# Kernel optimization log

Measured on AMD Instinct MI355X. Metric: run time of the kernel, lower is better.

## Reference

```python
import jax, jax.numpy as jnp
import numpy as np

V, C, H, L, E, D, B, T = 32000, 1024, 16, 3, 8, 1024, 8, 512
FF = 4 * C
EPS = 1e-5


def setup_inputs() -> dict:
    key = jax.random.key(0)
    ks = iter(jax.random.split(key, 32))
    def w(shape, s=0.02):
        return jax.random.normal(next(ks), shape, jnp.float32) * s
    return {
        "idx": jax.random.randint(next(ks), (B, T), 0, V),
        "tok_emb": w((V, C)),
        "ln1_g": jnp.ones((L, C)), "ln1_b": jnp.zeros((L, C)),
        "ln2_g": jnp.ones((L, C)), "ln2_b": jnp.zeros((L, C)),
        "qkv_w": w((L, C, 3 * C)), "proj_w": w((L, C, C)),
        "ff_w1": w((L, C, FF)), "ff_b1": jnp.zeros((L, FF)),
        "ff_w2": w((L, FF, C)), "ff_b2": jnp.zeros((L, C)),
        "router_w": w((C, E)),
        "exp_w1": w((E, C, D)), "exp_b1": jnp.zeros((E, D)),
        "exp_w2": w((E, D, C)), "exp_b2": jnp.zeros((E, C)),
        "lnf_g": jnp.ones((C,)), "lnf_b": jnp.zeros((C,)),
        "head_w": w((C, V)),
    }


def layernorm(x, g, b):
    m = x.mean(-1, keepdims=True)
    v = x.var(-1, keepdims=True)
    return (x - m) * jax.lax.rsqrt(v + EPS) * g + b


def rope_cos_sin(t, d):
    inv = 1.0 / (10000.0 ** (jnp.arange(0, d, 2, dtype=jnp.float32) / d))
    fr = jnp.arange(t, dtype=jnp.float32)[:, None] * inv[None, :]  # [T, d/2]
    emb = jnp.concatenate([fr, fr], -1)  # [T, d]
    return jnp.cos(emb), jnp.sin(emb)


def rot_half(x):
    x1, x2 = jnp.split(x, 2, axis=-1)
    return jnp.concatenate([-x2, x1], -1)


def attn(x, qkv_w, proj_w):
    b, t, c = x.shape
    d = c // H
    qkv = (x @ qkv_w).reshape(b, t, 3, H, d).transpose(2, 0, 3, 1, 4)  # [3,B,H,T,d]
    q, k, v = qkv[0], qkv[1], qkv[2]
    cos, sin = rope_cos_sin(t, d)
    q = q * cos + rot_half(q) * sin
    k = k * cos + rot_half(k) * sin
    s = jnp.einsum('bhqd,bhkd->bhqk', q, k) / np.float32(np.sqrt(d))
    causal = jnp.tril(jnp.ones((t, t), bool))
    s = jnp.where(causal, s, jnp.float32(-1e30))
    a = jax.nn.softmax(s, -1)
    y = jnp.einsum('bhqk,bhkd->bhqd', a, v)
    y = y.transpose(0, 2, 1, 3).reshape(b, t, c)
    return y @ proj_w


def moe(xf, router_w, exp_w1, exp_b1, exp_w2, exp_b2):
    # router softmax -> top-2 -> renormalize -> scatter into dense [N,E] mask
    probs = jax.nn.softmax(xf @ router_w, -1)
    tw, ti = jax.lax.top_k(probs, 2)
    tw = tw / tw.sum(-1, keepdims=True)
    n = xf.shape[0]
    mask = jnp.zeros((n, E), xf.dtype).at[jnp.arange(n)[:, None], ti].set(tw)
    # per-expert dense FFN over all tokens, combined with sparse weights
    h = jax.nn.gelu(jnp.einsum('nc,ecd->end', xf, exp_w1) + exp_b1[:, None, :], approximate=False)
    y = jnp.einsum('end,edc->enc', h, exp_w2) + exp_b2[:, None, :]
    return jnp.einsum('ne,enc->nc', mask, y)


def reference(idx, tok_emb, ln1_g, ln1_b, ln2_g, ln2_b, qkv_w, proj_w,
              ff_w1, ff_b1, ff_w2, ff_b2, router_w, exp_w1, exp_b1,
              exp_w2, exp_b2, lnf_g, lnf_b, head_w):
    x = tok_emb[idx]  # [B,T,C]
    for l in range(L):
        x = x + attn(layernorm(x, ln1_g[l], ln1_b[l]), qkv_w[l], proj_w[l])
        h = layernorm(x, ln2_g[l], ln2_b[l])
        x = x + (jax.nn.gelu(h @ ff_w1[l] + ff_b1[l], approximate=False) @ ff_w2[l] + ff_b2[l])
    b, t, c = x.shape
    x = moe(x.reshape(b * t, c), router_w, exp_w1, exp_b1, exp_w2, exp_b2).reshape(b, t, c)
    x = layernorm(x, lnf_g, lnf_b)
    return x @ head_w  # logits [B,T,V]
```

## Files before the change

kernel.cpp:

```cpp
#include <hip/hip_runtime.h>
#include <math.h>


#define NTOK  4096
#define CDIM  1024
#define HEADS 16
#define DHEAD 64
#define LAYERS 3
#define NEXP  8
#define DEXP  1024
#define TSEQ  512
#define FFDIM 4096
#define VOCAB 32000
#define C3    3072

typedef __attribute__((ext_vector_type(8))) short short8;
typedef __attribute__((ext_vector_type(4))) float f32x4;

__device__ __forceinline__ unsigned short f2bf(float f) {
  unsigned int u = __builtin_bit_cast(unsigned int, f);
  return (unsigned short)((u + 0x7fffu + ((u >> 16) & 1u)) >> 16);
}
__device__ __forceinline__ float bf2f(unsigned short h) {
  return __builtin_bit_cast(float, ((unsigned int)h) << 16);
}

__global__ __launch_bounds__(256) void embed_kernel(const int* __restrict__ idx,
                                                    const float* __restrict__ emb,
                                                    float* __restrict__ x) {
  int i = blockIdx.x * 256 + threadIdx.x;
  int n = i >> 8, c4 = i & 255;
  const float4* src = (const float4*)(emb + (size_t)idx[n] * CDIM);
  ((float4*)(x + (size_t)n * CDIM))[c4] = src[c4];
}

__global__ void rope_table_kernel(float* __restrict__ ct, float* __restrict__ st) {
  int t = blockIdx.x, p = threadIdx.x;
  float inv = powf(10000.0f, -(float)p / 32.0f);
  float ang = (float)t * inv;
  ct[t * 32 + p] = cosf(ang);
  st[t * 32 + p] = sinf(ang);
}

__global__ __launch_bounds__(256) void qkv_prep_kernel(
    const float* __restrict__ qkv, const float* __restrict__ ct,
    const float* __restrict__ st,
    unsigned short* __restrict__ Qh, unsigned short* __restrict__ Qm,
    unsigned short* __restrict__ Ql,
    unsigned short* __restrict__ Kh, unsigned short* __restrict__ Km,
    unsigned short* __restrict__ Kl,
    unsigned short* __restrict__ Vth, unsigned short* __restrict__ Vtm,
    unsigned short* __restrict__ Vtl) {
  __shared__ unsigned short sVh[64 * 64], sVm[64 * 64], sVl[64 * 64];
  const int tid = threadIdx.x;
  const int tt0 = blockIdx.x * 64, h = blockIdx.y, b = blockIdx.z;
  const int bh = b * HEADS + h;
#pragma unroll
  for (int u = 0; u < 8; u++) {
    int pidx = tid + u * 256;
    int tl = pidx >> 5, p = pidx & 31;
    int t = tt0 + tl;
    size_t nb = ((size_t)(b * TSEQ + t)) * C3 + h * DHEAD;
    float c0 = ct[t * 32 + p], s0 = st[t * 32 + p];
    size_t ob = ((size_t)bh * TSEQ + t) * 64;
    float a = qkv[nb + p], bb = qkv[nb + p + 32];
    float lo = a * c0 - bb * s0, hi = bb * c0 + a * s0;
    unsigned short w0, w1;
    float r;
    w0 = f2bf(lo); r = lo - bf2f(w0); w1 = f2bf(r); r -= bf2f(w1);
    Qh[ob + p] = w0; Qm[ob + p] = w1; Ql[ob + p] = f2bf(r);
    w0 = f2bf(hi); r = hi - bf2f(w0); w1 = f2bf(r); r -= bf2f(w1);
    Qh[ob + p + 32] = w0; Qm[ob + p + 32] = w1; Ql[ob + p + 32] = f2bf(r);
    a = qkv[nb + CDIM + p]; bb = qkv[nb + CDIM + p + 32];
    lo = a * c0 - bb * s0; hi = bb * c0 + a * s0;
    w0 = f2bf(lo); r = lo - bf2f(w0); w1 = f2bf(r); r -= bf2f(w1);
    Kh[ob + p] = w0; Km[ob + p] = w1; Kl[ob + p] = f2bf(r);
    w0 = f2bf(hi); r = hi - bf2f(w0); w1 = f2bf(r); r -= bf2f(w1);
    Kh[ob + p + 32] = w0; Km[ob + p + 32] = w1; Kl[ob + p + 32] = f2bf(r);
  }
#pragma unroll
  for (int u = 0; u < 4; u++) {
    int vidx = tid + u * 256;
    int tl = vidx >> 4, d4 = (vidx & 15) * 4;
    int t = tt0 + tl;
    float4 v = *(const float4*)(qkv + ((size_t)(b * TSEQ + t)) * C3 + 2 * CDIM + h * DHEAD + d4);
    float vv[4] = {v.x, v.y, v.z, v.w};
#pragma unroll
    for (int j = 0; j < 4; j++) {
      unsigned short w0 = f2bf(vv[j]);
      float r = vv[j] - bf2f(w0);
      unsigned short w1 = f2bf(r);
      r -= bf2f(w1);
      sVh[(d4 + j) * 64 + tl] = w0;
      sVm[(d4 + j) * 64 + tl] = w1;
      sVl[(d4 + j) * 64 + tl] = f2bf(r);
    }
  }
  __syncthreads();
#pragma unroll
  for (int u = 0; u < 2; u++) {
    int idx = tid + u * 256;
    int d = idx >> 3, seg = (idx & 7) * 8;
    size_t go = ((size_t)bh * 64 + d) * TSEQ + tt0 + seg;
    *(short8*)(Vth + go) = *(const short8*)(sVh + d * 64 + seg);
    *(short8*)(Vtm + go) = *(const short8*)(sVm + d * 64 + seg);
    *(short8*)(Vtl + go) = *(const short8*)(sVl + d * 64 + seg);
  }
}

__global__ __launch_bounds__(256) void flash_attn_kernel(
    const unsigned short* __restrict__ Qh, const unsigned short* __restrict__ Qm,
    const unsigned short* __restrict__ Ql,
    const unsigned short* __restrict__ Kh, const unsigned short* __restrict__ Km,
    const unsigned short* __restrict__ Kl,
    const unsigned short* __restrict__ Vth, const unsigned short* __restrict__ Vtm,
    const unsigned short* __restrict__ Vtl,
    unsigned short* __restrict__ ath, unsigned short* __restrict__ atl) {
  __shared__ __align__(16) unsigned short sK[3][2][64 * 32];
  __shared__ __align__(16) unsigned short sV[3][2][64 * 32];
  __shared__ __align__(16) unsigned short sP[3][2][4][16 * 32];
  const int tid = threadIdx.x;
  const int wv = tid >> 6, ln = tid & 63;
  const int qt = blockIdx.x, h = blockIdx.y, b = blockIdx.z;
  const int bh = b * HEADS + h;
  const int lr = ln & 15, lg = ln >> 4;
  const int q0 = qt * 64 + wv * 16;

  const size_t qoff = ((size_t)bh * TSEQ + q0 + lr) * 64 + 8 * lg;
  short8 qf[3][2];
  qf[0][0] = *(const short8*)(Qh + qoff); qf[0][1] = *(const short8*)(Qh + qoff + 32);
  qf[1][0] = *(const short8*)(Qm + qoff); qf[1][1] = *(const short8*)(Qm + qoff + 32);
  qf[2][0] = *(const short8*)(Ql + qoff); qf[2][1] = *(const short8*)(Ql + qoff + 32);

  f32x4 Y[4];
#pragma unroll
  for (int j = 0; j < 4; j++) Y[j] = (f32x4){0.f, 0.f, 0.f, 0.f};
  float m[4] = {-1e30f, -1e30f, -1e30f, -1e30f};
  float l[4] = {0.f, 0.f, 0.f, 0.f};

  const int r0 = tid >> 3, sg = (tid & 7) * 8;
  const int half = sg >> 5, soff = (sg & 31);

  for (int kt = 0; kt <= qt; kt++) {
    const int kb = kt * 64;
    short8 stg[12];
#pragma unroll
    for (int u = 0; u < 2; u++) {
      int row = r0 + 32 * u;
      size_t gk = ((size_t)bh * TSEQ + kb + row) * 64 + sg;
      size_t gv = ((size_t)bh * 64 + row) * TSEQ + kb + sg;
      stg[u * 6 + 0] = *(const short8*)(Kh + gk);
      stg[u * 6 + 1] = *(const short8*)(Km + gk);
      stg[u * 6 + 2] = *(const short8*)(Kl + gk);
      stg[u * 6 + 3] = *(const short8*)(Vth + gv);
      stg[u * 6 + 4] = *(const short8*)(Vtm + gv);
      stg[u * 6 + 5] = *(const short8*)(Vtl + gv);
    }
    __syncthreads();
#pragma unroll
    for (int u = 0; u < 2; u++) {
      int off = (r0 + 32 * u) * 32 + soff;
      *(short8*)(&sK[0][half][off]) = stg[u * 6 + 0];
      *(short8*)(&sK[1][half][off]) = stg[u * 6 + 1];
      *(short8*)(&sK[2][half][off]) = stg[u * 6 + 2];
      *(short8*)(&sV[0][half][off]) = stg[u * 6 + 3];
      *(short8*)(&sV[1][half][off]) = stg[u * 6 + 4];
      *(short8*)(&sV[2][half][off]) = stg[u * 6 + 5];
    }
    __syncthreads();

    f32x4 s[4];
#pragma unroll
    for (int j = 0; j < 4; j++) s[j] = (f32x4){0.f, 0.f, 0.f, 0.f};
#pragma unroll
    for (int j = 0; j < 4; j++) {
      const int ko = (16 * j + lr) * 32 + 8 * lg;
      short8 k0[3], k1[3];
#pragma unroll
      for (int lv = 0; lv < 3; lv++) {
        k0[lv] = *(const short8*)(&sK[lv][0][ko]);
        k1[lv] = *(const short8*)(&sK[lv][1][ko]);
      }
      s[j] = __builtin_amdgcn_mfma_f32_16x16x32_bf16(qf[0][0], k0[0], s[j], 0, 0, 0);
      s[j] = __builtin_amdgcn_mfma_f32_16x16x32_bf16(qf[0][1], k1[0], s[j], 0, 0, 0);
      s[j] = __builtin_amdgcn_mfma_f32_16x16x32_bf16(qf[0][0], k0[1], s[j], 0, 0, 0);
      s[j] = __builtin_amdgcn_mfma_f32_16x16x32_bf16(qf[0][1], k1[1], s[j], 0, 0, 0);
      s[j] = __builtin_amdgcn_mfma_f32_16x16x32_bf16(qf[1][0], k0[0], s[j], 0, 0, 0);
      s[j] = __builtin_amdgcn_mfma_f32_16x16x32_bf16(qf[1][1], k1[0], s[j], 0, 0, 0);
      s[j] = __builtin_amdgcn_mfma_f32_16x16x32_bf16(qf[0][0], k0[2], s[j], 0, 0, 0);
      s[j] = __builtin_amdgcn_mfma_f32_16x16x32_bf16(qf[0][1], k1[2], s[j], 0, 0, 0);
      s[j] = __builtin_amdgcn_mfma_f32_16x16x32_bf16(qf[1][0], k0[1], s[j], 0, 0, 0);
      s[j] = __builtin_amdgcn_mfma_f32_16x16x32_bf16(qf[1][1], k1[1], s[j], 0, 0, 0);
      s[j] = __builtin_amdgcn_mfma_f32_16x16x32_bf16(qf[2][0], k0[0], s[j], 0, 0, 0);
      s[j] = __builtin_amdgcn_mfma_f32_16x16x32_bf16(qf[2][1], k1[0], s[j], 0, 0, 0);
    }

    const bool diag = (kt == qt);
#pragma unroll
    for (int rr = 0; rr < 4; rr++) {
      const int q = q0 + 4 * lg + rr;
      float mx = -1e30f;
#pragma unroll
      for (int j = 0; j < 4; j++) {
        float v = s[j][rr] * 0.125f;
        if (diag && (kb + 16 * j + lr > q)) v = -1e30f;
        s[j][rr] = v;
        mx = fmaxf(mx, v);
      }
      mx = fmaxf(mx, __shfl_xor(mx, 1));
      mx = fmaxf(mx, __shfl_xor(mx, 2));
      mx = fmaxf(mx, __shfl_xor(mx, 4));
      mx = fmaxf(mx, __shfl_xor(mx, 8));
      float mn = fmaxf(m[rr], mx);
      float al = expf(m[rr] - mn);
      m[rr] = mn;
      l[rr] *= al;
#pragma unroll
      for (int j = 0; j < 4; j++) Y[j][rr] *= al;
      float ps = 0.f;
#pragma unroll
      for (int j = 0; j < 4; j++) {
        float p = expf(s[j][rr] - mn);
        s[j][rr] = p;
        ps += p;
      }
      l[rr] += ps;
    }

#pragma unroll
    for (int j = 0; j < 4; j++) {
      const int jh = j >> 1;
      const int col = 16 * (j & 1) + lr;
#pragma unroll
      for (int rr = 0; rr < 4; rr++) {
        float p = s[j][rr];
        unsigned short w0 = f2bf(p);
        float r = p - bf2f(w0);
        unsigned short w1 = f2bf(r);
        r -= bf2f(w1);
        const int o = (4 * lg + rr) * 32 + col;
        sP[0][jh][wv][o] = w0;
        sP[1][jh][wv][o] = w1;
        sP[2][jh][wv][o] = f2bf(r);
      }
    }
    __syncthreads();
    const int po = lr * 32 + 8 * lg;
    short8 pf[3][2];
#pragma unroll
    for (int lv = 0; lv < 3; lv++) {
      pf[lv][0] = *(const short8*)(&sP[lv][0][wv][po]);
      pf[lv][1] = *(const short8*)(&sP[lv][1][wv][po]);
    }
#pragma unroll
    for (int jd = 0; jd < 4; jd++) {
      const int vo = (16 * jd + lr) * 32 + 8 * lg;
      short8 v0[3], v1[3];
#pragma unroll
      for (int lv = 0; lv < 3; lv++) {
        v0[lv] = *(const short8*)(&sV[lv][0][vo]);
        v1[lv] = *(const short8*)(&sV[lv][1][vo]);
      }
      Y[jd] = __builtin_amdgcn_mfma_f32_16x16x32_bf16(pf[0][0], v0[0], Y[jd], 0, 0, 0);
      Y[jd] = __builtin_amdgcn_mfma_f32_16x16x32_bf16(pf[0][1], v1[0], Y[jd], 0, 0, 0);
      Y[jd] = __builtin_amdgcn_mfma_f32_16x16x32_bf16(pf[0][0], v0[1], Y[jd], 0, 0, 0);
      Y[jd] = __builtin_amdgcn_mfma_f32_16x16x32_bf16(pf[0][1], v1[1], Y[jd], 0, 0, 0);
      Y[jd] = __builtin_amdgcn_mfma_f32_16x16x32_bf16(pf[1][0], v0[0], Y[jd], 0, 0, 0);
      Y[jd] = __builtin_amdgcn_mfma_f32_16x16x32_bf16(pf[1][1], v1[0], Y[jd], 0, 0, 0);
      Y[jd] = __builtin_amdgcn_mfma_f32_16x16x32_bf16(pf[0][0], v0[2], Y[jd], 0, 0, 0);
      Y[jd] = __builtin_amdgcn_mfma_f32_16x16x32_bf16(pf[0][1], v1[2], Y[jd], 0, 0, 0);
      Y[jd] = __builtin_amdgcn_mfma_f32_16x16x32_bf16(pf[1][0], v0[1], Y[jd], 0, 0, 0);
      Y[jd] = __builtin_amdgcn_mfma_f32_16x16x32_bf16(pf[1][1], v1[1], Y[jd], 0, 0, 0);
      Y[jd] = __builtin_amdgcn_mfma_f32_16x16x32_bf16(pf[2][0], v0[0], Y[jd], 0, 0, 0);
      Y[jd] = __builtin_amdgcn_mfma_f32_16x16x32_bf16(pf[2][1], v1[0], Y[jd], 0, 0, 0);
    }
  }

#pragma unroll
  for (int rr = 0; rr < 4; rr++) {
    float t = l[rr];
    t += __shfl_xor(t, 1); t += __shfl_xor(t, 2);
    t += __shfl_xor(t, 4); t += __shfl_xor(t, 8);
    l[rr] = 1.0f / t;
  }
#pragma unroll
  for (int jd = 0; jd < 4; jd++) {
    const int d = 16 * jd + lr;
#pragma unroll
    for (int rr = 0; rr < 4; rr++) {
      const int q = q0 + 4 * lg + rr;
      float v = Y[jd][rr] * l[rr];
      unsigned short w0 = f2bf(v);
      const size_t ci = ((size_t)(b * TSEQ + q)) * CDIM + h * DHEAD + d;
      ath[ci] = w0;
      atl[ci] = f2bf(v - bf2f(w0));
    }
  }
}

__global__ __launch_bounds__(256) void ln_split_kernel(const float* __restrict__ x,
                                                       unsigned short* __restrict__ yh,
                                                       unsigned short* __restrict__ yl,
                                                       const float* __restrict__ g,
                                                       const float* __restrict__ b) {
  int n = blockIdx.x, tid = threadIdx.x;
  const float4* xr = (const float4*)(x + (size_t)n * CDIM);
  float4 v = xr[tid];
  float s = v.x + v.y + v.z + v.w;
  float ss = v.x * v.x + v.y * v.y + v.z * v.z + v.w * v.w;
  __shared__ float rs[256], rss[256];
  rs[tid] = s; rss[tid] = ss;
  __syncthreads();
  for (int o = 128; o > 0; o >>= 1) {
    if (tid < o) { rs[tid] += rs[tid + o]; rss[tid] += rss[tid + o]; }
    __syncthreads();
  }
  float m = rs[0] * (1.0f / CDIM);
  float var = rss[0] * (1.0f / CDIM) - m * m;
  float r = rsqrtf(var + 1e-5f);
  float4 gv = ((const float4*)g)[tid];
  float4 bv = ((const float4*)b)[tid];
  float o0 = (v.x - m) * r * gv.x + bv.x;
  float o1 = (v.y - m) * r * gv.y + bv.y;
  float o2 = (v.z - m) * r * gv.z + bv.z;
  float o3 = (v.w - m) * r * gv.w + bv.w;
  ushort4 hh, ll;
  hh.x = f2bf(o0); ll.x = f2bf(o0 - bf2f(hh.x));
  hh.y = f2bf(o1); ll.y = f2bf(o1 - bf2f(hh.y));
  hh.z = f2bf(o2); ll.z = f2bf(o2 - bf2f(hh.z));
  hh.w = f2bf(o3); ll.w = f2bf(o3 - bf2f(hh.w));
  ((ushort4*)(yh + (size_t)n * CDIM))[tid] = hh;
  ((ushort4*)(yl + (size_t)n * CDIM))[tid] = ll;
}

__global__ __launch_bounds__(256) void cvt_bf16_kernel(const float* __restrict__ x,
                                                       unsigned short* __restrict__ y) {
  int i = blockIdx.x * 256 + threadIdx.x;
  float4 v = ((const float4*)x)[i];
  ushort4 o;
  o.x = f2bf(v.x); o.y = f2bf(v.y); o.z = f2bf(v.z); o.w = f2bf(v.w);
  ((ushort4*)y)[i] = o;
}

__global__ __launch_bounds__(256) void ln_bf16_kernel(const float* __restrict__ x,
                                                      unsigned short* __restrict__ y,
                                                      const float* __restrict__ g,
                                                      const float* __restrict__ b) {
  int n = blockIdx.x, tid = threadIdx.x;
  const float4* xr = (const float4*)(x + (size_t)n * CDIM);
  float4 v = xr[tid];
  float s = v.x + v.y + v.z + v.w;
  float ss = v.x * v.x + v.y * v.y + v.z * v.z + v.w * v.w;
  __shared__ float rs[256], rss[256];
  rs[tid] = s; rss[tid] = ss;
  __syncthreads();
  for (int o = 128; o > 0; o >>= 1) {
    if (tid < o) { rs[tid] += rs[tid + o]; rss[tid] += rss[tid + o]; }
    __syncthreads();
  }
  float m = rs[0] * (1.0f / CDIM);
  float var = rss[0] * (1.0f / CDIM) - m * m;
  float r = rsqrtf(var + 1e-5f);
  float4 gv = ((const float4*)g)[tid];
  float4 bv = ((const float4*)b)[tid];
  ushort4 o4;
  o4.x = f2bf((v.x - m) * r * gv.x + bv.x);
  o4.y = f2bf((v.y - m) * r * gv.y + bv.y);
  o4.z = f2bf((v.z - m) * r * gv.z + bv.z);
  o4.w = f2bf((v.w - m) * r * gv.w + bv.w);
  ((ushort4*)(y + (size_t)n * CDIM))[tid] = o4;
}

__global__ __launch_bounds__(256) void wconv_t_kernel(const float* __restrict__ W,
                                                      unsigned short* __restrict__ Wt,
                                                      int K, int N) {
  __shared__ float t[32][33];
  int n0 = blockIdx.x * 32, k0 = blockIdx.y * 32;
  int tx = threadIdx.x & 31, ty = threadIdx.x >> 5;
#pragma unroll
  for (int i = 0; i < 4; i++)
    t[ty + 8 * i][tx] = W[(size_t)(k0 + ty + 8 * i) * N + n0 + tx];
  __syncthreads();
#pragma unroll
  for (int i = 0; i < 4; i++)
    Wt[(size_t)(n0 + ty + 8 * i) * K + k0 + tx] = f2bf(t[tx][ty + 8 * i]);
}

__global__ __launch_bounds__(256) void wconv_split_kernel(const float* __restrict__ W,
                                                          unsigned short* __restrict__ Wh,
                                                          unsigned short* __restrict__ Wl,
                                                          int K, int N) {
  __shared__ float t[32][33];
  int n0 = blockIdx.x * 32, k0 = blockIdx.y * 32;
  int tx = threadIdx.x & 31, ty = threadIdx.x >> 5;
#pragma unroll
  for (int i = 0; i < 4; i++)
    t[ty + 8 * i][tx] = W[(size_t)(k0 + ty + 8 * i) * N + n0 + tx];
  __syncthreads();
#pragma unroll
  for (int i = 0; i < 4; i++) {
    float w = t[tx][ty + 8 * i];
    unsigned short h = f2bf(w);
    size_t o = (size_t)(n0 + ty + 8 * i) * K + k0 + tx;
    Wh[o] = h;
    Wl[o] = f2bf(w - bf2f(h));
  }
}

__device__ __forceinline__ void xcd_swz(int& bx, int& by) {
  int bid = blockIdx.y * gridDim.x + blockIdx.x;
  int cpx = (gridDim.x * gridDim.y) >> 3;
  bid = (bid & 7) * cpx + (bid >> 3);
  bx = bid % gridDim.x;
  by = bid / gridDim.x;
}

template <int MODE>
__global__ __launch_bounds__(256) void gemm_split(const unsigned short* __restrict__ Ah,
                                                  const unsigned short* __restrict__ Al,
                                                  const unsigned short* __restrict__ Bth,
                                                  const unsigned short* __restrict__ Btl,
                                                  float* __restrict__ C,
                                                  unsigned short* __restrict__ Ch,
                                                  unsigned short* __restrict__ Cl,
                                                  const float* __restrict__ bias,
                                                  int M, int Nn, int K) {
  __shared__ __align__(16) unsigned short AsH[128 * 32];
  __shared__ __align__(16) unsigned short AsL[128 * 32];
  __shared__ __align__(16) unsigned short BsH[128 * 32];
  __shared__ __align__(16) unsigned short BsL[128 * 32];
  const int tid = threadIdx.x;
  const int wv = tid >> 6, ln = tid & 63;
  int sbx, sby;
  xcd_swz(sbx, sby);
  const int bm = sby * 128, bn = sbx * 128;

  const size_t aoff0 = (size_t)(bm + 32 * wv + (ln >> 2)) * K + (size_t)((ln & 3) * 8);
  const size_t aoff1 = aoff0 + (size_t)16 * K;
  const size_t boff0 = (size_t)(bn + 32 * wv + (ln >> 2)) * K + (size_t)((ln & 3) * 8);
  const size_t boff1 = boff0 + (size_t)16 * K;
  const int lofs = 1024 * wv + ln * 8;

  const int wm = wv >> 1, wn = wv & 1;
  const int lr = ln & 15, lg = ln >> 4;

  f32x4 acc[4][4];
#pragma unroll
  for (int i = 0; i < 4; i++)
#pragma unroll
    for (int j = 0; j < 4; j++) acc[i][j] = (f32x4){0.f, 0.f, 0.f, 0.f};

  for (int k0 = 0; k0 < K; k0 += 32) {
    short8 rah0 = *(const short8*)(Ah + aoff0 + k0);
    short8 rah1 = *(const short8*)(Ah + aoff1 + k0);
    short8 ral0 = *(const short8*)(Al + aoff0 + k0);
    short8 ral1 = *(const short8*)(Al + aoff1 + k0);
    short8 rbh0 = *(const short8*)(Bth + boff0 + k0);
    short8 rbh1 = *(const short8*)(Bth + boff1 + k0);
    short8 rbl0 = *(const short8*)(Btl + boff0 + k0);
    short8 rbl1 = *(const short8*)(Btl + boff1 + k0);
    __syncthreads();
    *(short8*)(AsH + lofs)       = rah0;
    *(short8*)(AsH + lofs + 512) = rah1;
    *(short8*)(AsL + lofs)       = ral0;
    *(short8*)(AsL + lofs + 512) = ral1;
    *(short8*)(BsH + lofs)       = rbh0;
    *(short8*)(BsH + lofs + 512) = rbh1;
    *(short8*)(BsL + lofs)       = rbl0;
    *(short8*)(BsL + lofs + 512) = rbl1;
    __syncthreads();

    short8 afh[4], afl[4], bwh[4], bwl[4];
#pragma unroll
    for (int i = 0; i < 4; i++) {
      const int ao = (64 * wm + 16 * i + lr) * 32 + 8 * lg;
      afh[i] = *(const short8*)(AsH + ao);
      afl[i] = *(const short8*)(AsL + ao);
    }
#pragma unroll
    for (int j = 0; j < 4; j++) {
      const int bo = (64 * wn + 16 * j + lr) * 32 + 8 * lg;
      bwh[j] = *(const short8*)(BsH + bo);
      bwl[j] = *(const short8*)(BsL + bo);
    }
#pragma unroll
    for (int i = 0; i < 4; i++)
#pragma unroll
      for (int j = 0; j < 4; j++) {
        acc[i][j] = __builtin_amdgcn_mfma_f32_16x16x32_bf16(afh[i], bwh[j], acc[i][j], 0, 0, 0);
        acc[i][j] = __builtin_amdgcn_mfma_f32_16x16x32_bf16(afl[i], bwh[j], acc[i][j], 0, 0, 0);
        acc[i][j] = __builtin_amdgcn_mfma_f32_16x16x32_bf16(afh[i], bwl[j], acc[i][j], 0, 0, 0);
      }
  }

#pragma unroll
  for (int j = 0; j < 4; j++) {
    const int n = bn + 64 * wn + 16 * j + lr;
    const float bb = (MODE == 1 || MODE == 3) ? bias[n] : 0.0f;
#pragma unroll
    for (int i = 0; i < 4; i++) {
#pragma unroll
      for (int rr = 0; rr < 4; rr++) {
        const int m = bm + 64 * wm + 16 * i + 4 * lg + rr;
        float v = acc[i][j][rr];
        const size_t ci = (size_t)m * Nn + n;
        if constexpr (MODE == 0) {
          C[ci] = v;
        } else if constexpr (MODE == 1) {
          v += bb;
          v = 0.5f * v * (1.0f + erff(v * 0.70710678118654752f));
          unsigned short h = f2bf(v);
          Ch[ci] = h;
          Cl[ci] = f2bf(v - bf2f(h));
        } else if constexpr (MODE == 2) {
          C[ci] += v;
        } else {
          C[ci] += v + bb;
        }
      }
    }
  }
}

__global__ __launch_bounds__(256) void gemm_bf16(const unsigned short* __restrict__ A,
                                                 const unsigned short* __restrict__ Bt,
                                                 float* __restrict__ C,
                                                 int M, int Nn, int K) {
  __shared__ __align__(16) unsigned short As[128 * 32];
  __shared__ __align__(16) unsigned short Bs[128 * 32];
  const int tid = threadIdx.x;
  const int wv = tid >> 6, ln = tid & 63;
  int sbx, sby;
  xcd_swz(sbx, sby);
  const int bm = sby * 128, bn = sbx * 128;

  const size_t aoff0 = (size_t)(bm + 32 * wv + (ln >> 2)) * K + (size_t)((ln & 3) * 8);
  const size_t aoff1 = aoff0 + (size_t)16 * K;
  const size_t boff0 = (size_t)(bn + 32 * wv + (ln >> 2)) * K + (size_t)((ln & 3) * 8);
  const size_t boff1 = boff0 + (size_t)16 * K;
  const int lofs = 1024 * wv + ln * 8;

  const int wm = wv >> 1, wn = wv & 1;
  const int lr = ln & 15, lg = ln >> 4;

  f32x4 acc[4][4];
#pragma unroll
  for (int i = 0; i < 4; i++)
#pragma unroll
    for (int j = 0; j < 4; j++) acc[i][j] = (f32x4){0.f, 0.f, 0.f, 0.f};

  for (int k0 = 0; k0 < K; k0 += 32) {
    short8 ra0 = *(const short8*)(A + aoff0 + k0);
    short8 ra1 = *(const short8*)(A + aoff1 + k0);
    short8 rb0 = *(const short8*)(Bt + boff0 + k0);
    short8 rb1 = *(const short8*)(Bt + boff1 + k0);
    __syncthreads();
    *(short8*)(As + lofs)       = ra0;
    *(short8*)(As + lofs + 512) = ra1;
    *(short8*)(Bs + lofs)       = rb0;
    *(short8*)(Bs + lofs + 512) = rb1;
    __syncthreads();

    short8 af[4], bw[4];
#pragma unroll
    for (int i = 0; i < 4; i++)
      af[i] = *(const short8*)(As + ((64 * wm + 16 * i + lr) * 32 + 8 * lg));
#pragma unroll
    for (int j = 0; j < 4; j++)
      bw[j] = *(const short8*)(Bs + ((64 * wn + 16 * j + lr) * 32 + 8 * lg));
#pragma unroll
    for (int i = 0; i < 4; i++)
#pragma unroll
      for (int j = 0; j < 4; j++)
        acc[i][j] = __builtin_amdgcn_mfma_f32_16x16x32_bf16(af[i], bw[j], acc[i][j], 0, 0, 0);
  }

#pragma unroll
  for (int j = 0; j < 4; j++) {
    const int n = bn + 64 * wn + 16 * j + lr;
#pragma unroll
    for (int i = 0; i < 4; i++) {
#pragma unroll
      for (int r = 0; r < 4; r++) {
        const int m = bm + 64 * wm + 16 * i + 4 * lg + r;
        C[(size_t)m * Nn + n] = acc[i][j][r];
      }
    }
  }
}

__global__ __launch_bounds__(256) void gemm_moe1(const unsigned short* __restrict__ A,
                                                 const unsigned short* __restrict__ Bt,
                                                 unsigned short* __restrict__ Cu,
                                                 const float* __restrict__ bias,
                                                 const int* __restrict__ cnt,
                                                 const int* __restrict__ lst,
                                                 int Nn, int K) {
  const int ce = *cnt;
  const int bm = blockIdx.y * 128, bn = blockIdx.x * 128;
  if (bm >= ce) return;
  __shared__ __align__(16) unsigned short As[128 * 32];
  __shared__ __align__(16) unsigned short Bs[128 * 32];
  const int tid = threadIdx.x;
  const int wv = tid >> 6, ln = tid & 63;

  const int ra = bm + 32 * wv + (ln >> 2);
  const int t0 = lst[(ra      < ce) ? ra      : 0];
  const int t1 = lst[(ra + 16 < ce) ? ra + 16 : 0];
  const size_t aoff0 = (size_t)t0 * K + (size_t)((ln & 3) * 8);
  const size_t aoff1 = (size_t)t1 * K + (size_t)((ln & 3) * 8);
  const size_t boff0 = (size_t)(bn + 32 * wv + (ln >> 2)) * K + (size_t)((ln & 3) * 8);
  const size_t boff1 = boff0 + (size_t)16 * K;
  const int lofs = 1024 * wv + ln * 8;

  const int wm = wv >> 1, wn = wv & 1;
  const int lr = ln & 15, lg = ln >> 4;

  f32x4 acc[4][4];
#pragma unroll
  for (int i = 0; i < 4; i++)
#pragma unroll
    for (int j = 0; j < 4; j++) acc[i][j] = (f32x4){0.f, 0.f, 0.f, 0.f};

  for (int k0 = 0; k0 < K; k0 += 32) {
    short8 ra0 = *(const short8*)(A + aoff0 + k0);
    short8 ra1 = *(const short8*)(A + aoff1 + k0);
    short8 rb0 = *(const short8*)(Bt + boff0 + k0);
    short8 rb1 = *(const short8*)(Bt + boff1 + k0);
    __syncthreads();
    *(short8*)(As + lofs)       = ra0;
    *(short8*)(As + lofs + 512) = ra1;
    *(short8*)(Bs + lofs)       = rb0;
    *(short8*)(Bs + lofs + 512) = rb1;
    __syncthreads();

    short8 af[4], bw[4];
#pragma unroll
    for (int i = 0; i < 4; i++)
      af[i] = *(const short8*)(As + ((64 * wm + 16 * i + lr) * 32 + 8 * lg));
#pragma unroll
    for (int j = 0; j < 4; j++)
      bw[j] = *(const short8*)(Bs + ((64 * wn + 16 * j + lr) * 32 + 8 * lg));
#pragma unroll
    for (int i = 0; i < 4; i++)
#pragma unroll
      for (int j = 0; j < 4; j++)
        acc[i][j] = __builtin_amdgcn_mfma_f32_16x16x32_bf16(af[i], bw[j], acc[i][j], 0, 0, 0);
  }

#pragma unroll
  for (int j = 0; j < 4; j++) {
    const int n = bn + 64 * wn + 16 * j + lr;
    const float bb = bias[n];
#pragma unroll
    for (int i = 0; i < 4; i++) {
#pragma unroll
      for (int r = 0; r < 4; r++) {
        const int m = bm + 64 * wm + 16 * i + 4 * lg + r;
        float v = acc[i][j][r] + bb;
        v = 0.5f * v * (1.0f + erff(v * 0.70710678118654752f));
        Cu[(size_t)m * Nn + n] = f2bf(v);
      }
    }
  }
}

__global__ __launch_bounds__(256) void gemm_moe2(const unsigned short* __restrict__ A,
                                                 const unsigned short* __restrict__ Bt,
                                                 float* __restrict__ C,
                                                 const float* __restrict__ bias,
                                                 const int* __restrict__ cnt,
                                                 const int* __restrict__ lst,
                                                 const float* __restrict__ wts,
                                                 int Nn, int K) {
  const int ce = *cnt;
  const int bm = blockIdx.y * 128, bn = blockIdx.x * 128;
  if (bm >= ce) return;
  __shared__ __align__(16) unsigned short As[128 * 32];
  __shared__ __align__(16) unsigned short Bs[128 * 32];
  const int tid = threadIdx.x;
  const int wv = tid >> 6, ln = tid & 63;

  const size_t aoff0 = (size_t)(bm + 32 * wv + (ln >> 2)) * K + (size_t)((ln & 3) * 8);
  const size_t aoff1 = aoff0 + (size_t)16 * K;
  const size_t boff0 = (size_t)(bn + 32 * wv + (ln >> 2)) * K + (size_t)((ln & 3) * 8);
  const size_t boff1 = boff0 + (size_t)16 * K;
  const int lofs = 1024 * wv + ln * 8;

  const int wm = wv >> 1, wn = wv & 1;
  const int lr = ln & 15, lg = ln >> 4;

  f32x4 acc[4][4];
#pragma unroll
  for (int i = 0; i < 4; i++)
#pragma unroll
    for (int j = 0; j < 4; j++) acc[i][j] = (f32x4){0.f, 0.f, 0.f, 0.f};

  for (int k0 = 0; k0 < K; k0 += 32) {
    short8 ra0 = *(const short8*)(A + aoff0 + k0);
    short8 ra1 = *(const short8*)(A + aoff1 + k0);
    short8 rb0 = *(const short8*)(Bt + boff0 + k0);
    short8 rb1 = *(const short8*)(Bt + boff1 + k0);
    __syncthreads();
    *(short8*)(As + lofs)       = ra0;
    *(short8*)(As + lofs + 512) = ra1;
    *(short8*)(Bs + lofs)       = rb0;
    *(short8*)(Bs + lofs + 512) = rb1;
    __syncthreads();

    short8 af[4], bw[4];
#pragma unroll
    for (int i = 0; i < 4; i++)
      af[i] = *(const short8*)(As + ((64 * wm + 16 * i + lr) * 32 + 8 * lg));
#pragma unroll
    for (int j = 0; j < 4; j++)
      bw[j] = *(const short8*)(Bs + ((64 * wn + 16 * j + lr) * 32 + 8 * lg));
#pragma unroll
    for (int i = 0; i < 4; i++)
#pragma unroll
      for (int j = 0; j < 4; j++)
        acc[i][j] = __builtin_amdgcn_mfma_f32_16x16x32_bf16(af[i], bw[j], acc[i][j], 0, 0, 0);
  }

#pragma unroll
  for (int j = 0; j < 4; j++) {
    const int n = bn + 64 * wn + 16 * j + lr;
    const float bb = bias[n];
#pragma unroll
    for (int i = 0; i < 4; i++) {
#pragma unroll
      for (int r = 0; r < 4; r++) {
        const int m = bm + 64 * wm + 16 * i + 4 * lg + r;
        if (m < ce) {
          const int tok = lst[m];
          C[(size_t)tok * Nn + n] += wts[m] * (acc[i][j][r] + bb);
        }
      }
    }
  }
}

__global__ __launch_bounds__(64) void router2_kernel(const float* __restrict__ x,
                                                     const float* __restrict__ rw,
                                                     int* __restrict__ cnt,
                                                     int* __restrict__ lst,
                                                     float* __restrict__ wts) {
  int n = blockIdx.x, lane = threadIdx.x;
  const float* xr = x + (size_t)n * CDIM;
  float acc[NEXP] = {};
  for (int i = 0; i < CDIM / 64; i++) {
    int c = lane + 64 * i;
    float xv = xr[c];
    const float* r = rw + (size_t)c * NEXP;
#pragma unroll
    for (int e = 0; e < NEXP; e++) acc[e] += xv * r[e];
  }
  for (int m = 32; m >= 1; m >>= 1)
#pragma unroll
    for (int e = 0; e < NEXP; e++) acc[e] += __shfl_xor(acc[e], m);
  if (lane == 0) {
    float mx = acc[0];
#pragma unroll
    for (int e = 1; e < NEXP; e++) mx = fmaxf(mx, acc[e]);
    float p[NEXP];
#pragma unroll
    for (int e = 0; e < NEXP; e++) p[e] = expf(acc[e] - mx);
    int i1 = 0;
#pragma unroll
    for (int e = 1; e < NEXP; e++) if (p[e] > p[i1]) i1 = e;
    int i2 = (i1 == 0) ? 1 : 0;
#pragma unroll
    for (int e = 0; e < NEXP; e++) if (e != i1 && p[e] > p[i2]) i2 = e;
    float denom = p[i1] + p[i2];
    int p1 = atomicAdd(&cnt[i1], 1);
    lst[i1 * NTOK + p1] = n;
    wts[i1 * NTOK + p1] = p[i1] / denom;
    int p2 = atomicAdd(&cnt[i2], 1);
    lst[i2 * NTOK + p2] = n;
    wts[i2 * NTOK + p2] = p[i2] / denom;
  }
}

extern "C" void kernel_launch(void* const* d_in, const int* in_sizes, int n_in,
                              void* d_out, int out_size, void* d_ws, size_t ws_size,
                              hipStream_t stream) {
  const int*   idx      = (const int*)d_in[0];
  const float* tok_emb  = (const float*)d_in[1];
  const float* ln1_g    = (const float*)d_in[2];
  const float* ln1_b    = (const float*)d_in[3];
  const float* ln2_g    = (const float*)d_in[4];
  const float* ln2_b    = (const float*)d_in[5];
  const float* qkv_w    = (const float*)d_in[6];
  const float* proj_w   = (const float*)d_in[7];
  const float* ff_w1    = (const float*)d_in[8];
  const float* ff_b1    = (const float*)d_in[9];
  const float* ff_w2    = (const float*)d_in[10];
  const float* ff_b2    = (const float*)d_in[11];
  const float* router_w = (const float*)d_in[12];
  const float* exp_w1   = (const float*)d_in[13];
  const float* exp_b1   = (const float*)d_in[14];
  const float* exp_w2   = (const float*)d_in[15];
  const float* exp_b2   = (const float*)d_in[16];
  const float* lnf_g    = (const float*)d_in[17];
  const float* lnf_b    = (const float*)d_in[18];
  const float* head_w   = (const float*)d_in[19];
  float* out = (float*)d_out;

  const size_t NC = (size_t)NTOK * CDIM;
  char* w = (char*)d_ws;
  float* x  = (float*)w;                 w += NC * 4;
  unsigned short* S1 = (unsigned short*)w; w += NC * 4;
  float* Q  = (float*)w;                 w += (size_t)NTOK * C3 * 4;
  float* C3r = (float*)w;                w += NC * 4;
  unsigned short* WS = (unsigned short*)w; w += NC * 4;
  unsigned short* EX = (unsigned short*)w; w += NC * 6;
  float* ct = (float*)w;                 w += (size_t)TSEQ * 32 * 4;
  float* st = (float*)w;                 w += (size_t)TSEQ * 32 * 4;
  int*   moe_cnt = (int*)w;              w += NEXP * 4;
  int*   moe_lst = (int*)w;              w += (size_t)NEXP * NTOK * 4;
  float* moe_wts = (float*)w;            w += (size_t)NEXP * NTOK * 4;

  unsigned short* xh = S1;
  unsigned short* xl = S1 + NC;
  unsigned short* Wh = WS;
  unsigned short* Wl = WS + NC;
  float* qkvf = Q;
  unsigned short* Qh_s = S1;
  unsigned short* Qm_s = S1 + NC;
  unsigned short* Ql_s = EX;
  unsigned short* Kh_s = (unsigned short*)C3r;
  unsigned short* Km_s = (unsigned short*)C3r + NC;
  unsigned short* Kl_s = EX + NC;
  unsigned short* Vth_s = WS;
  unsigned short* Vtm_s = WS + NC;
  unsigned short* Vtl_s = EX + 2 * NC;
  unsigned short* ath = (unsigned short*)Q;
  unsigned short* atl = (unsigned short*)Q + NC;
  unsigned short* hh = (unsigned short*)Q;
  unsigned short* hl = (unsigned short*)Q + (size_t)NTOK * FFDIM;
  unsigned short* x_bf    = S1;
  unsigned short* hmoe_bf = S1 + NC;
  float* moe_out  = x;
  unsigned short* wt_s = WS;
  unsigned short* xn_bf   = S1;
  unsigned short* wt_head = (unsigned short*)Q;

  embed_kernel<<<NTOK, 256, 0, stream>>>(idx, tok_emb, x);
  rope_table_kernel<<<TSEQ, 32, 0, stream>>>(ct, st);

  for (int l = 0; l < LAYERS; l++) {
    ln_split_kernel<<<NTOK, 256, 0, stream>>>(x, xh, xl, ln1_g + l * CDIM, ln1_b + l * CDIM);
    wconv_split_kernel<<<dim3(C3 / 32, CDIM / 32), 256, 0, stream>>>(
        qkv_w + (size_t)l * CDIM * C3, Wh, Wl, CDIM, C3);
    gemm_split<0><<<dim3(C3 / 128, NTOK / 128), 256, 0, stream>>>(
        xh, xl, Wh, Wl, qkvf, nullptr, nullptr, nullptr, NTOK, C3, CDIM);
    qkv_prep_kernel<<<dim3(TSEQ / 64, HEADS, 8), 256, 0, stream>>>(
        qkvf, ct, st, Qh_s, Qm_s, Ql_s, Kh_s, Km_s, Kl_s, Vth_s, Vtm_s, Vtl_s);
    flash_attn_kernel<<<dim3(TSEQ / 64, HEADS, 8), 256, 0, stream>>>(
        Qh_s, Qm_s, Ql_s, Kh_s, Km_s, Kl_s, Vth_s, Vtm_s, Vtl_s, ath, atl);
    wconv_split_kernel<<<dim3(CDIM / 32, CDIM / 32), 256, 0, stream>>>(
        proj_w + (size_t)l * CDIM * CDIM, Wh, Wl, CDIM, CDIM);
    gemm_split<2><<<dim3(CDIM / 128, NTOK / 128), 256, 0, stream>>>(
        ath, atl, Wh, Wl, x, nullptr, nullptr, nullptr, NTOK, CDIM, CDIM);
    ln_split_kernel<<<NTOK, 256, 0, stream>>>(x, xh, xl, ln2_g + l * CDIM, ln2_b + l * CDIM);
    wconv_split_kernel<<<dim3(FFDIM / 32, CDIM / 32), 256, 0, stream>>>(
        ff_w1 + (size_t)l * CDIM * FFDIM, Wh, Wl, CDIM, FFDIM);
    gemm_split<1><<<dim3(FFDIM / 128, NTOK / 128), 256, 0, stream>>>(
        xh, xl, Wh, Wl, nullptr, hh, hl, ff_b1 + (size_t)l * FFDIM, NTOK, FFDIM, CDIM);
    wconv_split_kernel<<<dim3(CDIM / 32, FFDIM / 32), 256, 0, stream>>>(
        ff_w2 + (size_t)l * FFDIM * CDIM, Wh, Wl, FFDIM, CDIM);
    gemm_split<3><<<dim3(CDIM / 128, NTOK / 128), 256, 0, stream>>>(
        hh, hl, Wh, Wl, x, nullptr, nullptr, ff_b2 + (size_t)l * CDIM, NTOK, CDIM, FFDIM);
  }

  hipMemsetAsync(moe_cnt, 0, NEXP * sizeof(int), stream);
  router2_kernel<<<NTOK, 64, 0, stream>>>(x, router_w, moe_cnt, moe_lst, moe_wts);
  cvt_bf16_kernel<<<(NC / 4) / 256, 256, 0, stream>>>(x, x_bf);
  hipMemsetAsync(moe_out, 0, NC * sizeof(float), stream);
  for (int e = 0; e < NEXP; e++) {
    wconv_t_kernel<<<dim3(DEXP / 32, CDIM / 32), 256, 0, stream>>>(
        exp_w1 + (size_t)e * CDIM * DEXP, wt_s, CDIM, DEXP);
    gemm_moe1<<<dim3(DEXP / 128, NTOK / 128), 256, 0, stream>>>(
        x_bf, wt_s, hmoe_bf, exp_b1 + (size_t)e * DEXP,
        moe_cnt + e, moe_lst + (size_t)e * NTOK, DEXP, CDIM);
    wconv_t_kernel<<<dim3(CDIM / 32, DEXP / 32), 256, 0, stream>>>(
        exp_w2 + (size_t)e * DEXP * CDIM, wt_s, DEXP, CDIM);
    gemm_moe2<<<dim3(CDIM / 128, NTOK / 128), 256, 0, stream>>>(
        hmoe_bf, wt_s, moe_out, exp_b2 + (size_t)e * CDIM,
        moe_cnt + e, moe_lst + (size_t)e * NTOK, moe_wts + (size_t)e * NTOK,
        CDIM, DEXP);
  }

  ln_bf16_kernel<<<NTOK, 256, 0, stream>>>(moe_out, xn_bf, lnf_g, lnf_b);
  wconv_t_kernel<<<dim3(VOCAB / 32, CDIM / 32), 256, 0, stream>>>(head_w, wt_head, CDIM, VOCAB);
  gemm_bf16<<<dim3(VOCAB / 128, NTOK / 128), 256, 0, stream>>>(
      xn_bf, wt_head, out, NTOK, VOCAB, CDIM);
}
```

Measured before the change: 3.038 ms.

## Batch all MoE experts into single grouped launches with atomic accumulation

Replaces the per-expert loop of weight conversion and two GEMMs with single launches that use blockIdx.z as the expert index. Each expert gets its own transposed weights and hidden-activation buffer, so the experts run concurrently instead of serialising. Because experts now overlap, the scatter into the output uses atomicAdd in place of a read-modify-write. This cuts launch count and fills the GPU better when per-expert token counts are small. The cost is larger scratch buffers and atomic traffic on the output, whose summation order is no longer fixed.

New measurement: 2.470 ms (median of 2 runs). -18.7%, faster.

```diff
diff --git a/kernel.cpp b/kernel.cpp
--- a/kernel.cpp
+++ b/kernel.cpp
@@ -373,8 +373,11 @@
 
 __global__ __launch_bounds__(256) void wconv_t_kernel(const float* __restrict__ W,
                                                       unsigned short* __restrict__ Wt,
-                                                      int K, int N) {
+                                                      int K, int N,
+                                                      size_t wstride, size_t ostride) {
   __shared__ float t[32][33];
+  W  += (size_t)blockIdx.z * wstride;
+  Wt += (size_t)blockIdx.z * ostride;
   int n0 = blockIdx.x * 32, k0 = blockIdx.y * 32;
   int tx = threadIdx.x & 31, ty = threadIdx.x >> 5;
 #pragma unroll
@@ -590,15 +593,21 @@
 }
 
 __global__ __launch_bounds__(256) void gemm_moe1(const unsigned short* __restrict__ A,
-                                                 const unsigned short* __restrict__ Bt,
-                                                 unsigned short* __restrict__ Cu,
-                                                 const float* __restrict__ bias,
-                                                 const int* __restrict__ cnt,
-                                                 const int* __restrict__ lst,
+                                                 const unsigned short* __restrict__ BtAll,
+                                                 unsigned short* __restrict__ CuAll,
+                                                 const float* __restrict__ biasAll,
+                                                 const int* __restrict__ cntAll,
+                                                 const int* __restrict__ lstAll,
                                                  int Nn, int K) {
-  const int ce = *cnt;
+  const int e = blockIdx.z;
+  const int ce = cntAll[e];
   const int bm = blockIdx.y * 128, bn = blockIdx.x * 128;
   if (bm >= ce) return;
+  const unsigned short* Bt = BtAll + (size_t)e * Nn * K;
+  unsigned short* Cu = CuAll + (size_t)e * NTOK * Nn;
+  const float* bias = biasAll + (size_t)e * Nn;
+  const int* lst = lstAll + (size_t)e * NTOK;
+
   __shared__ __align__(16) unsigned short As[128 * 32];
   __shared__ __align__(16) unsigned short Bs[128 * 32];
   const int tid = threadIdx.x;
@@ -665,17 +674,24 @@
   }
 }
 
-__global__ __launch_bounds__(256) void gemm_moe2(const unsigned short* __restrict__ A,
-                                                 const unsigned short* __restrict__ Bt,
+__global__ __launch_bounds__(256) void gemm_moe2(const unsigned short* __restrict__ AAll,
+                                                 const unsigned short* __restrict__ BtAll,
                                                  float* __restrict__ C,
-                                                 const float* __restrict__ bias,
-                                                 const int* __restrict__ cnt,
-                                                 const int* __restrict__ lst,
-                                                 const float* __restrict__ wts,
+                                                 const float* __restrict__ biasAll,
+                                                 const int* __restrict__ cntAll,
+                                                 const int* __restrict__ lstAll,
+                                                 const float* __restrict__ wtsAll,
                                                  int Nn, int K) {
-  const int ce = *cnt;
+  const int e = blockIdx.z;
+  const int ce = cntAll[e];
   const int bm = blockIdx.y * 128, bn = blockIdx.x * 128;
   if (bm >= ce) return;
+  const unsigned short* A = AAll + (size_t)e * NTOK * K;
+  const unsigned short* Bt = BtAll + (size_t)e * Nn * K;
+  const float* bias = biasAll + (size_t)e * Nn;
+  const int* lst = lstAll + (size_t)e * NTOK;
+  const float* wts = wtsAll + (size_t)e * NTOK;
+
   __shared__ __align__(16) unsigned short As[128 * 32];
   __shared__ __align__(16) unsigned short Bs[128 * 32];
   const int tid = threadIdx.x;
@@ -733,7 +749,7 @@
         const int m = bm + 64 * wm + 16 * i + 4 * lg + r;
         if (m < ce) {
           const int tok = lst[m];
-          C[(size_t)tok * Nn + n] += wts[m] * (acc[i][j][r] + bb);
+          atomicAdd(&C[(size_t)tok * Nn + n], wts[m] * (acc[i][j][r] + bb));
         }
       }
     }
@@ -838,10 +854,11 @@
   unsigned short* atl = (unsigned short*)Q + NC;
   unsigned short* hh = (unsigned short*)Q;
   unsigned short* hl = (unsigned short*)Q + (size_t)NTOK * FFDIM;
-  unsigned short* x_bf    = S1;
-  unsigned short* hmoe_bf = S1 + NC;
+  unsigned short* x_bf   = S1;
+  unsigned short* exp1t  = EX;
+  unsigned short* exp2t  = WS;
+  unsigned short* hmoeC  = (unsigned short*)Q;
   float* moe_out  = x;
-  unsigned short* wt_s = WS;
   unsigned short* xn_bf   = S1;
   unsigned short* wt_head = (unsigned short*)Q;
 
@@ -876,23 +893,19 @@
   hipMemsetAsync(moe_cnt, 0, NEXP * sizeof(int), stream);
   router2_kernel<<<NTOK, 64, 0, stream>>>(x, router_w, moe_cnt, moe_lst, moe_wts);
   cvt_bf16_kernel<<<(NC / 4) / 256, 256, 0, stream>>>(x, x_bf);
+  wconv_t_kernel<<<dim3(DEXP / 32, CDIM / 32, NEXP), 256, 0, stream>>>(
+      exp_w1, exp1t, CDIM, DEXP, (size_t)CDIM * DEXP, (size_t)CDIM * DEXP);
+  wconv_t_kernel<<<dim3(CDIM / 32, DEXP / 32, NEXP), 256, 0, stream>>>(
+      exp_w2, exp2t, DEXP, CDIM, (size_t)DEXP * CDIM, (size_t)DEXP * CDIM);
+  gemm_moe1<<<dim3(DEXP / 128, NTOK / 128, NEXP), 256, 0, stream>>>(
+      x_bf, exp1t, hmoeC, exp_b1, moe_cnt, moe_lst, DEXP, CDIM);
   hipMemsetAsync(moe_out, 0, NC * sizeof(float), stream);
-  for (int e = 0; e < NEXP; e++) {
-    wconv_t_kernel<<<dim3(DEXP / 32, CDIM / 32), 256, 0, stream>>>(
-        exp_w1 + (size_t)e * CDIM * DEXP, wt_s, CDIM, DEXP);
-    gemm_moe1<<<dim3(DEXP / 128, NTOK / 128), 256, 0, stream>>>(
-        x_bf, wt_s, hmoe_bf, exp_b1 + (size_t)e * DEXP,
-        moe_cnt + e, moe_lst + (size_t)e * NTOK, DEXP, CDIM);
-    wconv_t_kernel<<<dim3(CDIM / 32, DEXP / 32), 256, 0, stream>>>(
-        exp_w2 + (size_t)e * DEXP * CDIM, wt_s, DEXP, CDIM);
-    gemm_moe2<<<dim3(CDIM / 128, NTOK / 128), 256, 0, stream>>>(
-        hmoe_bf, wt_s, moe_out, exp_b2 + (size_t)e * CDIM,
-        moe_cnt + e, moe_lst + (size_t)e * NTOK, moe_wts + (size_t)e * NTOK,
-        CDIM, DEXP);
-  }
+  gemm_moe2<<<dim3(CDIM / 128, NTOK / 128, NEXP), 256, 0, stream>>>(
+      hmoeC, exp2t, moe_out, exp_b2, moe_cnt, moe_lst, moe_wts, CDIM, DEXP);
 
   ln_bf16_kernel<<<NTOK, 256, 0, stream>>>(moe_out, xn_bf, lnf_g, lnf_b);
-  wconv_t_kernel<<<dim3(VOCAB / 32, CDIM / 32), 256, 0, stream>>>(head_w, wt_head, CDIM, VOCAB);
+  wconv_t_kernel<<<dim3(VOCAB / 32, CDIM / 32, 1), 256, 0, stream>>>(
+      head_w, wt_head, CDIM, VOCAB, 0, 0);
   gemm_bf16<<<dim3(VOCAB / 128, NTOK / 128), 256, 0, stream>>>(
       xn_bf, wt_head, out, NTOK, VOCAB, CDIM);
 }
```
